# Kernel optimization log

Measured on AMD Instinct MI355X. Metric: run time of the kernel, lower is better.

The kernel has to match this reference:

```python
import jax, jax.numpy as jnp
import numpy as np

N, E, IN, ED, HID, HEADS, OUT, G = 50000, 800000, 128, 16, 32, 4, 64, 64
NEG_SLOPE = 0.2


def gat_conv(x, src, dst, edge_attr, W, att_src, att_dst, We, att_edge, bias,
             heads, out_ch, concat):
    """PyG-style GATConv with edge attributes and mean-filled self loops.
    src/dst already include self loops; edge_attr already includes fill rows."""
    n = x.shape[0]
    h = (x @ W).reshape(n, heads, out_ch)                      # [N,H,C]
    a_src = jnp.einsum('nhc,hc->nh', h, att_src)               # [N,H]
    a_dst = jnp.einsum('nhc,hc->nh', h, att_dst)
    eh = (edge_attr @ We).reshape(-1, heads, out_ch)           # [E',H,C]
    a_edge = jnp.einsum('ehc,hc->eh', eh, att_edge)            # [E',H]
    alpha = jax.nn.leaky_relu(a_src[src] + a_dst[dst] + a_edge, NEG_SLOPE)
    # segment softmax over incoming edges of each target node
    amax = jax.ops.segment_max(alpha, dst, num_segments=n)
    ex = jnp.exp(alpha - amax[dst])
    denom = jax.ops.segment_sum(ex, dst, num_segments=n)
    coef = ex / (denom[dst] + 1e-16)                           # [E',H]
    msg = h[src] * coef[:, :, None]                            # [E',H,C]
    out = jax.ops.segment_sum(msg, dst, num_segments=n)        # [N,H,C]
    out = out.reshape(n, heads * out_ch) if concat else out.mean(axis=1)
    return out + bias


def add_self_loops(edge_index, edge_attr, n):
    loop = jnp.arange(n, dtype=edge_index.dtype)
    src = jnp.concatenate([edge_index[0], loop])
    dst = jnp.concatenate([edge_index[1], loop])
    fill = jnp.broadcast_to(edge_attr.mean(axis=0), (n, edge_attr.shape[1]))
    ea = jnp.concatenate([edge_attr, fill], axis=0)
    return src, dst, ea


def setup_inputs() -> dict:
    key = jax.random.key(0)
    ks = jax.random.split(key, 16)
    s1 = 1.0 / np.sqrt(IN)
    s2 = 1.0 / np.sqrt(HID * HEADS)
    se = 1.0 / np.sqrt(ED)
    return {
        'x': jax.random.normal(ks[0], (N, IN), jnp.float32),
        'edge_index': jax.random.randint(ks[1], (2, E), 0, N, jnp.int64),
        'edge_attr': jax.random.normal(ks[2], (E, ED), jnp.float32),
        'batch': jnp.sort(jax.random.randint(ks[3], (N,), 0, G, jnp.int64)),
        # layer 1 params (heads=4, concat=True)
        'W1': jax.random.normal(ks[4], (IN, HEADS * HID), jnp.float32) * s1,
        'att_src1': jax.random.normal(ks[5], (HEADS, HID), jnp.float32) * s1,
        'att_dst1': jax.random.normal(ks[6], (HEADS, HID), jnp.float32) * s1,
        'We1': jax.random.normal(ks[7], (ED, HEADS * HID), jnp.float32) * se,
        'att_edge1': jax.random.normal(ks[8], (HEADS, HID), jnp.float32) * se,
        'b1': jnp.zeros((HEADS * HID,), jnp.float32),
        # layer 2 params (heads=1, concat=False)
        'W2': jax.random.normal(ks[9], (HEADS * HID, OUT), jnp.float32) * s2,
        'att_src2': jax.random.normal(ks[10], (1, OUT), jnp.float32) * s2,
        'att_dst2': jax.random.normal(ks[11], (1, OUT), jnp.float32) * s2,
        'We2': jax.random.normal(ks[12], (ED, OUT), jnp.float32) * se,
        'att_edge2': jax.random.normal(ks[13], (1, OUT), jnp.float32) * se,
        'b2': jnp.zeros((OUT,), jnp.float32),
    }


def reference(x, edge_index, edge_attr, batch,
              W1, att_src1, att_dst1, We1, att_edge1, b1,
              W2, att_src2, att_dst2, We2, att_edge2, b2):
    src, dst, ea = add_self_loops(edge_index, edge_attr, x.shape[0])
    h = gat_conv(x, src, dst, ea, W1, att_src1, att_dst1, We1, att_edge1, b1,
                 HEADS, HID, concat=True)
    h = jax.nn.elu(h)
    h = gat_conv(h, src, dst, ea, W2, att_src2, att_dst2, We2, att_edge2, b2,
                 1, OUT, concat=False)
    # global mean pool over graphs
    sums = jax.ops.segment_sum(h, batch, num_segments=G)
    cnts = jax.ops.segment_sum(jnp.ones((h.shape[0],), h.dtype), batch, num_segments=G)
    return sums / jnp.maximum(cnts, 1.0)[:, None]
```

## Files before the change

### kernel.cpp

```cpp
#include <hip/hip_runtime.h>
#include <hip/hip_fp16.h>
#include <math.h>

#define NN 50000
#define NE 800000
#define EDF 16
#define C1 128
#define HID 32
#define OUTF 64
#define NG 64
#define SLOPE 0.2f
#define NB 196
#define MAXE 256
#define PB 256
#define PCH 196
#define SEB 512
#define HB 3125
#define G1B 1563
#define G2B 1563

static inline int cdiv(long a, long b){ return (int)((a + b - 1) / b); }

__device__ __forceinline__ float lrelu(float x){ return x >= 0.f ? x : SLOPE * x; }

typedef _Float16 f16x8 __attribute__((ext_vector_type(8)));
typedef float f32x4 __attribute__((ext_vector_type(4)));
#define MFMA16(a, b, c) __builtin_amdgcn_mfma_f32_16x16x32_f16((a), (b), (c), 0, 0, 0)

__global__ __launch_bounds__(256) void k_pre(const float* __restrict__ ea,
                                             float* __restrict__ part,
                                             const int* __restrict__ dst,
                                             int* __restrict__ deg,
                                             int* __restrict__ rank){
  int b = blockIdx.x;
  int t = threadIdx.x;
  if (b < SEB){
    const float4* ea4 = (const float4*)ea;
    const long total = (long)NE * 4;
    const long stride = (long)SEB * 256;
    float4 acc = make_float4(0.f, 0.f, 0.f, 0.f);
    for (long i = (long)b * 256 + t; i < total; i += stride * 4){
      float4 a0 = make_float4(0,0,0,0), a1 = a0, a2 = a0, a3 = a0;
      long i1 = i + stride, i2 = i + 2*stride, i3 = i + 3*stride;
      a0 = ea4[i];
      if (i1 < total) a1 = ea4[i1];
      if (i2 < total) a2 = ea4[i2];
      if (i3 < total) a3 = ea4[i3];
      acc.x += a0.x + a1.x + a2.x + a3.x;
      acc.y += a0.y + a1.y + a2.y + a3.y;
      acc.z += a0.z + a1.z + a2.z + a3.z;
      acc.w += a0.w + a1.w + a2.w + a3.w;
    }
    __shared__ float4 sp[256];
    sp[t] = acc;
    __syncthreads();
    for (int st = 128; st >= 4; st >>= 1){
      if (t < st){
        sp[t].x += sp[t+st].x; sp[t].y += sp[t+st].y;
        sp[t].z += sp[t+st].z; sp[t].w += sp[t+st].w;
      }
      __syncthreads();
    }
    if (t < 4) *(float4*)&part[b * 16 + t * 4] = sp[t];
  } else {
    long e = (long)(b - SEB) * 256 + t;
    if (e < NE) rank[e] = atomicAdd(&deg[dst[e]], 1);
  }
}

__global__ void k_scan1(const int* __restrict__ deg, int* __restrict__ rowStart,
                        int* __restrict__ blockSums,
                        const float* __restrict__ We1, const float* __restrict__ att_e1,
                        const float* __restrict__ We2, const float* __restrict__ att_e2,
                        const float* __restrict__ part,
                        float* __restrict__ M1, float* __restrict__ M2,
                        float* __restrict__ aeSL1, float* __restrict__ aeSL2,
                        const float* __restrict__ W1, const float* __restrict__ W2,
                        __half* __restrict__ W1Th, __half* __restrict__ W1Tl,
                        __half* __restrict__ W2Th, __half* __restrict__ W2Tl){
  int t = threadIdx.x;
  if (blockIdx.x == NB + 1){
    for (int i = t; i < 128 * 128; i += 256){
      int c = i & 127, k = i >> 7;
      float w = W1[i];
      __half h = __float2half_rn(w);
      W1Th[c * 128 + k] = h;
      W1Tl[c * 128 + k] = __float2half_rn((w - __half2float(h)) * 4096.0f);
    }
    return;
  }
  if (blockIdx.x == NB + 2){
    for (int i = t; i < 128 * 64; i += 256){
      int c = i & 63, k = i >> 6;
      float w = W2[i];
      __half h = __float2half_rn(w);
      W2Th[c * 128 + k] = h;
      W2Tl[c * 128 + k] = __float2half_rn((w - __half2float(h)) * 4096.0f);
    }
    return;
  }
  if (blockIdx.x == NB){
    __shared__ float sMean[16];
    __shared__ float sM1p[64];
    if (t < 64){
      int h = t >> 4, d = t & 15;
      float s = 0.f;
      for (int c = 0; c < HID; c++) s += We1[d * C1 + h * HID + c] * att_e1[h * HID + c];
      M1[h * 16 + d] = s; sM1p[t] = s;
    }
    __shared__ float sM2p[16];
    if (t >= 64 && t < 80){
      int d = t - 64;
      float s = 0.f;
      for (int c = 0; c < OUTF; c++) s += We2[d * OUTF + c] * att_e2[c];
      M2[d] = s; sM2p[d] = s;
    }
    if (t >= 80 && t < 96){
      int c = t - 80;
      float s = 0.f;
      for (int b = 0; b < SEB; b++) s += part[b * 16 + c];
      sMean[c] = s * (1.0f / NE);
    }
    __syncthreads();
    if (t < 4){
      float s = 0.f;
      for (int d = 0; d < 16; d++) s += sMean[d] * sM1p[t * 16 + d];
      aeSL1[t] = s;
    }
    if (t == 4){
      float s = 0.f;
      for (int d = 0; d < 16; d++) s += sMean[d] * sM2p[d];
      *aeSL2 = s;
    }
    return;
  }
  __shared__ int sd[256];
  int i = blockIdx.x * 256 + t;
  int v = (i < NN) ? deg[i] : 0;
  sd[t] = v;
  __syncthreads();
  for (int off = 1; off < 256; off <<= 1){
    int add = (t >= off) ? sd[t - off] : 0;
    __syncthreads();
    sd[t] += add;
    __syncthreads();
  }
  int incl = sd[t];
  if (i < NN) rowStart[i] = incl - v;
  if (t == 255) blockSums[blockIdx.x] = incl;
}

__global__ void k_scan3(int* __restrict__ rowStart, const int* __restrict__ blockSums){
  __shared__ int sp[256];
  int t = threadIdx.x;
  int bid = blockIdx.x;
  sp[t] = (t < bid) ? blockSums[t] : 0;
  __syncthreads();
  for (int st = 128; st >= 1; st >>= 1){
    if (t < st) sp[t] += sp[t + st];
    __syncthreads();
  }
  int prefix = sp[0];
  int i = bid * 256 + t;
  if (i < NN) rowStart[i] += prefix;
  if (i == 0) rowStart[NN] = NE;
}

__global__ __launch_bounds__(256) void k_gemm1(
    const float* __restrict__ x,
    const __half* __restrict__ W1Th, const __half* __restrict__ W1Tl,
    __half* __restrict__ Ch,
    const float* __restrict__ attS, const float* __restrict__ attD,
    float* __restrict__ aS, float* __restrict__ aD){
  __shared__ __align__(16) __half Ash[4096];
  __shared__ __align__(16) __half Asl[4096];
  int t = threadIdx.x;
  int row0 = blockIdx.x * 32;
  {
    int srow = t >> 3, sseg = t & 7;
    int gr = row0 + srow;
    float xv[16];
    if (gr < NN){
      const float4* xp = (const float4*)(x + (long)gr * 128 + sseg * 16);
      *(float4*)&xv[0]  = xp[0]; *(float4*)&xv[4]  = xp[1];
      *(float4*)&xv[8]  = xp[2]; *(float4*)&xv[12] = xp[3];
    } else {
#pragma unroll
      for (int i = 0; i < 16; i++) xv[i] = 0.f;
    }
    f16x8 vh[2], vl[2];
#pragma unroll
    for (int q = 0; q < 2; q++)
#pragma unroll
      for (int i = 0; i < 8; i++){
        float f = xv[q * 8 + i];
        _Float16 h = (_Float16)f;
        vh[q][i] = h;
        vl[q][i] = (_Float16)(f - (float)h);
      }
    int sb = srow * 256 + sseg * 32;
    int sw = (srow & 7) << 4;
    *(f16x8*)((char*)Ash + ((sb     ) ^ sw)) = vh[0];
    *(f16x8*)((char*)Ash + ((sb + 16) ^ sw)) = vh[1];
    *(f16x8*)((char*)Asl + ((sb     ) ^ sw)) = vl[0];
    *(f16x8*)((char*)Asl + ((sb + 16) ^ sw)) = vl[1];
  }
  __syncthreads();
  int wave = t >> 6, lane = t & 63, g = lane >> 4, li = lane & 15;
  const f16x8* BhP = (const f16x8*)W1Th;
  const f16x8* BlP = (const f16x8*)W1Tl;
  int c0 = wave * 32 + li;
  int c1 = c0 + 16;
  f32x4 z = {0.f, 0.f, 0.f, 0.f};
  f32x4 aM00 = z, aM01 = z, aM10 = z, aM11 = z;
  f32x4 aL00 = z, aL01 = z, aL10 = z, aL11 = z;
  int ro0 = li * 256, ro1 = (16 + li) * 256;
  int sw0 = (li & 7) << 4;
#pragma unroll
  for (int ks = 0; ks < 4; ks++){
    int ko = ks * 64 + g * 16;
    f16x8 ah0 = *(const f16x8*)((char*)Ash + ((ro0 + ko) ^ sw0));
    f16x8 ah1 = *(const f16x8*)((char*)Ash + ((ro1 + ko) ^ sw0));
    f16x8 al0 = *(const f16x8*)((char*)Asl + ((ro0 + ko) ^ sw0));
    f16x8 al1 = *(const f16x8*)((char*)Asl + ((ro1 + ko) ^ sw0));
    f16x8 bh0 = BhP[c0 * 16 + ks * 4 + g];
    f16x8 bh1 = BhP[c1 * 16 + ks * 4 + g];
    f16x8 bl0 = BlP[c0 * 16 + ks * 4 + g];
    f16x8 bl1 = BlP[c1 * 16 + ks * 4 + g];
    aM00 = MFMA16(ah0, bh0, aM00); aM01 = MFMA16(ah0, bh1, aM01);
    aM10 = MFMA16(ah1, bh0, aM10); aM11 = MFMA16(ah1, bh1, aM11);
    aM00 = MFMA16(al0, bh0, aM00); aM01 = MFMA16(al0, bh1, aM01);
    aM10 = MFMA16(al1, bh0, aM10); aM11 = MFMA16(al1, bh1, aM11);
    aL00 = MFMA16(ah0, bl0, aL00); aL01 = MFMA16(ah0, bl1, aL01);
    aL10 = MFMA16(ah1, bl0, aL10); aL11 = MFMA16(ah1, bl1, aL11);
  }
  const float s = 1.0f / 4096.0f;
  f32x4 D00 = aM00 + aL00 * s, D01 = aM01 + aL01 * s;
  f32x4 D10 = aM10 + aL10 * s, D11 = aM11 + aL11 * s;
  float avS0 = attS[c0], avS1 = attS[c1];
  float avD0 = attD[c0], avD1 = attD[c1];
  float ssv[2][4], sdv[2][4];
#pragma unroll
  for (int r = 0; r < 4; r++){
    ssv[0][r] = D00[r] * avS0 + D01[r] * avS1;
    ssv[1][r] = D10[r] * avS0 + D11[r] * avS1;
    sdv[0][r] = D00[r] * avD0 + D01[r] * avD1;
    sdv[1][r] = D10[r] * avD0 + D11[r] * avD1;
  }
#pragma unroll
  for (int off = 1; off <= 8; off <<= 1)
#pragma unroll
    for (int mt = 0; mt < 2; mt++)
#pragma unroll
      for (int r = 0; r < 4; r++){
        ssv[mt][r] += __shfl_xor(ssv[mt][r], off);
        sdv[mt][r] += __shfl_xor(sdv[mt][r], off);
      }
  __syncthreads();
  __half* sOut = Ash;
#pragma unroll
  for (int mt = 0; mt < 2; mt++)
#pragma unroll
    for (int r = 0; r < 4; r++){
      int rl = mt * 16 + g * 4 + r;
      sOut[rl * 128 + c0] = __float2half_rn(mt ? D10[r] : D00[r]);
      sOut[rl * 128 + c1] = __float2half_rn(mt ? D11[r] : D01[r]);
    }
  if (li == 0){
#pragma unroll
    for (int mt = 0; mt < 2; mt++)
#pragma unroll
      for (int r = 0; r < 4; r++){
        int grow = row0 + mt * 16 + g * 4 + r;
        if (grow < NN){
          aS[(long)grow * 4 + wave] = ssv[mt][r];
          aD[(long)grow * 4 + wave] = sdv[mt][r];
        }
      }
  }
  __syncthreads();
  {
    int row = t >> 3, seg = t & 7;
    int grw = row0 + row;
    if (grw < NN){
      uint4 u0 = *(uint4*)&sOut[row * 128 + seg * 16];
      uint4 u1 = *(uint4*)&sOut[row * 128 + seg * 16 + 8];
      *(uint4*)&Ch[(long)grw * 128 + seg * 16] = u0;
      *(uint4*)&Ch[(long)grw * 128 + seg * 16 + 8] = u1;
    }
  }
}

__global__ __launch_bounds__(256) void k_sc(
    const int* __restrict__ src, const int* __restrict__ dst,
    const float* __restrict__ ea, const int* __restrict__ rowStart,
    const int* __restrict__ rank,
    const float* __restrict__ M1, const float* __restrict__ M2,
    unsigned int* __restrict__ recC){
  __shared__ float sM[80];
  int t = threadIdx.x;
  if (t < 64) sM[t] = M1[t];
  if (t >= 64 && t < 80) sM[t] = M2[t - 64];
  __syncthreads();
  long e = (long)blockIdx.x * 256 + t;
  if (e >= NE) return;
  int d = dst[e];
  int s = src[e];
  int rk = rank[e];
  float eav[16];
  const float4* p = (const float4*)(ea + e * EDF);
  *(float4*)&eav[0]  = p[0]; *(float4*)&eav[4]  = p[1];
  *(float4*)&eav[8]  = p[2]; *(float4*)&eav[12] = p[3];
  int pos = rowStart[d] + rk;
  float ae[4];
#pragma unroll
  for (int h = 0; h < 4; h++){
    float sdot = 0.f;
#pragma unroll
    for (int dd = 0; dd < 16; dd++) sdot += eav[dd] * sM[h * 16 + dd];
    ae[h] = sdot;
  }
  float a2 = 0.f;
#pragma unroll
  for (int dd = 0; dd < 16; dd++) a2 += eav[dd] * sM[64 + dd];
  __half2 ae01 = __floats2half2_rn(ae[0], ae[1]);
  __half2 ae23 = __floats2half2_rn(ae[2], ae[3]);
  __half  a2h  = __float2half_rn(a2);
  uint4 rec;
  rec.x = (unsigned)s | ((unsigned)*(unsigned short*)&a2h << 16);
  rec.y = *(unsigned*)&ae01;
  rec.z = *(unsigned*)&ae23;
  rec.w = 0u;
  *(uint4*)&recC[(long)pos * 4] = rec;
}

__global__ __launch_bounds__(256) void k_gemm2(
    const __half* __restrict__ Ahp,
    const __half* __restrict__ W2Th, const __half* __restrict__ W2Tl,
    __half* __restrict__ Ch,
    const float* __restrict__ attS, const float* __restrict__ attD,
    float* __restrict__ aS, float* __restrict__ aD){
  __shared__ __align__(16) __half As[4096];
  __shared__ float sRS[128], sRD[128];
  int t = threadIdx.x;
  int row0 = blockIdx.x * 32;
  {
    int srow = t >> 3, sseg = t & 7;
    int gr = row0 + srow;
    uint4 u0 = {0,0,0,0}, u1 = {0,0,0,0};
    if (gr < NN){
      const uint4* p = (const uint4*)(Ahp + (long)gr * 128 + sseg * 16);
      u0 = p[0]; u1 = p[1];
    }
    int sb = srow * 256 + sseg * 32;
    int sw = (srow & 7) << 4;
    *(uint4*)((char*)As + ((sb     ) ^ sw)) = u0;
    *(uint4*)((char*)As + ((sb + 16) ^ sw)) = u1;
  }
  __syncthreads();
  int wave = t >> 6, lane = t & 63, g = lane >> 4, li = lane & 15;
  int cw = wave * 16 + li;
  const f16x8* BhP = (const f16x8*)W2Th;
  const f16x8* BlP = (const f16x8*)W2Tl;
  f32x4 z = {0.f, 0.f, 0.f, 0.f};
  f32x4 aM0 = z, aM1 = z, aL0 = z, aL1 = z;
  int ro0 = li * 256, ro1 = (16 + li) * 256, sw0 = (li & 7) << 4;
#pragma unroll
  for (int ks = 0; ks < 4; ks++){
    int ko = ks * 64 + g * 16;
    f16x8 a0 = *(const f16x8*)((char*)As + ((ro0 + ko) ^ sw0));
    f16x8 a1 = *(const f16x8*)((char*)As + ((ro1 + ko) ^ sw0));
    f16x8 bh = BhP[cw * 16 + ks * 4 + g];
    f16x8 bl = BlP[cw * 16 + ks * 4 + g];
    aM0 = MFMA16(a0, bh, aM0); aM1 = MFMA16(a1, bh, aM1);
    aL0 = MFMA16(a0, bl, aL0); aL1 = MFMA16(a1, bl, aL1);
  }
  const float s = 1.0f / 4096.0f;
  f32x4 D0 = aM0 + aL0 * s, D1 = aM1 + aL1 * s;
  float avS = attS[cw], avD = attD[cw];
  float ssv[2][4], sdv[2][4];
#pragma unroll
  for (int r = 0; r < 4; r++){
    ssv[0][r] = D0[r] * avS; ssv[1][r] = D1[r] * avS;
    sdv[0][r] = D0[r] * avD; sdv[1][r] = D1[r] * avD;
  }
#pragma unroll
  for (int off = 1; off <= 8; off <<= 1)
#pragma unroll
    for (int mt = 0; mt < 2; mt++)
#pragma unroll
      for (int r = 0; r < 4; r++){
        ssv[mt][r] += __shfl_xor(ssv[mt][r], off);
        sdv[mt][r] += __shfl_xor(sdv[mt][r], off);
      }
  __syncthreads();
  __half* sOut = As;
#pragma unroll
  for (int mt = 0; mt < 2; mt++)
#pragma unroll
    for (int r = 0; r < 4; r++){
      int rl = mt * 16 + g * 4 + r;
      sOut[rl * 64 + cw] = __float2half_rn(mt ? D1[r] : D0[r]);
      if (li == 0){
        sRS[wave * 32 + rl] = ssv[mt][r];
        sRD[wave * 32 + rl] = sdv[mt][r];
      }
    }
  __syncthreads();
  if (t < 32){
    int grow = row0 + t;
    if (grow < NN){
      aS[grow] = sRS[t] + sRS[32 + t] + sRS[64 + t] + sRS[96 + t];
      aD[grow] = sRD[t] + sRD[32 + t] + sRD[64 + t] + sRD[96 + t];
    }
  }
  {
    int row = t >> 3, seg = t & 7;
    int grw = row0 + row;
    if (grw < NN)
      *(uint4*)&Ch[(long)grw * 64 + seg * 8] = *(uint4*)&sOut[row * 64 + seg * 8];
  }
}

__global__ __launch_bounds__(256) void k_agg1(
    const int* __restrict__ rowStart, const unsigned int* __restrict__ recC,
    const float* __restrict__ a_src, const float* __restrict__ a_dst,
    const float* __restrict__ aeSL1,
    const __half* __restrict__ h1h, const float* __restrict__ b1,
    __half* __restrict__ out1h){
  __shared__ int   sS[4][MAXE];
  __shared__ float sC[4][MAXE * 4];
  int wid = threadIdx.x >> 6;
  int lane = threadIdx.x & 63;
  int n = blockIdx.x * 4 + wid;
  int start = rowStart[n];
  int dg = rowStart[n + 1] - start;
  float4 sl4 = *(const float4*)aeSL1;
  float4 ad4 = *(const float4*)(a_dst + (long)n * 4);
  float4 as4 = *(const float4*)(a_src + (long)n * 4);
  float4 cSelf;
  cSelf.x = __expf(lrelu(as4.x + ad4.x + sl4.x));
  cSelf.y = __expf(lrelu(as4.y + ad4.y + sl4.y));
  cSelf.z = __expf(lrelu(as4.z + ad4.z + sl4.z));
  cSelf.w = __expf(lrelu(as4.w + ad4.w + sl4.w));
  float4 dsum = make_float4(0.f, 0.f, 0.f, 0.f);
  for (int j0 = 0; j0 < dg; j0 += 64){
    int j = j0 + lane;
    if (j < dg){
      uint4 rec = *(const uint4*)&recC[(long)(start + j) * 4];
      int s = rec.x & 0xffff;
      float2 ae01 = __half22float2(*(__half2*)&rec.y);
      float2 ae23 = __half22float2(*(__half2*)&rec.z);
      float4 asv = *(const float4*)(a_src + (long)s * 4);
      float4 c;
      c.x = __expf(lrelu(asv.x + ad4.x + ae01.x));
      c.y = __expf(lrelu(asv.y + ad4.y + ae01.y));
      c.z = __expf(lrelu(asv.z + ad4.z + ae23.x));
      c.w = __expf(lrelu(asv.w + ad4.w + ae23.y));
      dsum.x += c.x; dsum.y += c.y; dsum.z += c.z; dsum.w += c.w;
      if (j < MAXE){
        sS[wid][j] = s << 6;
        *(float4*)&sC[wid][j * 4] = c;
      }
    }
  }
#pragma unroll
  for (int off = 32; off > 0; off >>= 1){
    dsum.x += __shfl_xor(dsum.x, off);
    dsum.y += __shfl_xor(dsum.y, off);
    dsum.z += __shfl_xor(dsum.z, off);
    dsum.w += __shfl_xor(dsum.w, off);
  }
  float adA[4] = {ad4.x, ad4.y, ad4.z, ad4.w};
  float csA[4] = {cSelf.x, cSelf.y, cSelf.z, cSelf.w};
  float invA[4];
  invA[0] = 1.f / (dsum.x + cSelf.x + 1e-16f);
  invA[1] = 1.f / (dsum.y + cSelf.y + 1e-16f);
  invA[2] = 1.f / (dsum.z + cSelf.z + 1e-16f);
  invA[3] = 1.f / (dsum.w + cSelf.w + 1e-16f);
  int ch = lane * 2;
  int h = lane >> 4;
  const unsigned int* hrow = (const unsigned int*)h1h;
  float cs   = csA[h];
  float vinv = invA[h];
  float adh  = adA[h];
  unsigned int hv = hrow[(unsigned)(n * 64 + lane)];
  float2 hf = __half22float2(*(__half2*)&hv);
  float acc0 = hf.x * cs, acc1 = hf.y * cs;
  int jmax = dg < MAXE ? dg : MAXE;
  int j = 0;
  for (; j + 4 <= jmax; j += 4){
    int o0 = sS[wid][j+0], o1 = sS[wid][j+1], o2 = sS[wid][j+2], o3 = sS[wid][j+3];
    float c0 = sC[wid][(j+0)*4+h], c1 = sC[wid][(j+1)*4+h];
    float c2 = sC[wid][(j+2)*4+h], c3 = sC[wid][(j+3)*4+h];
    unsigned int v0 = hrow[(unsigned)(o0 + lane)];
    unsigned int v1 = hrow[(unsigned)(o1 + lane)];
    unsigned int v2 = hrow[(unsigned)(o2 + lane)];
    unsigned int v3 = hrow[(unsigned)(o3 + lane)];
    float2 f0 = __half22float2(*(__half2*)&v0);
    float2 f1 = __half22float2(*(__half2*)&v1);
    float2 f2 = __half22float2(*(__half2*)&v2);
    float2 f3 = __half22float2(*(__half2*)&v3);
    acc0 += c0 * f0.x + c1 * f1.x + c2 * f2.x + c3 * f3.x;
    acc1 += c0 * f0.y + c1 * f1.y + c2 * f2.y + c3 * f3.y;
  }
  for (; j < jmax; j++){
    int o = sS[wid][j];
    float c = sC[wid][j * 4 + h];
    unsigned int v = hrow[(unsigned)(o + lane)];
    float2 f = __half22float2(*(__half2*)&v);
    acc0 += c * f.x; acc1 += c * f.y;
  }
  for (; j < dg; j++){
    uint4 rec = *(const uint4*)&recC[(long)(start + j) * 4];
    int s = rec.x & 0xffff;
    float2 ae01 = __half22float2(*(__half2*)&rec.y);
    float2 ae23 = __half22float2(*(__half2*)&rec.z);
    float aeA[4] = {ae01.x, ae01.y, ae23.x, ae23.y};
    float asv = a_src[(long)s * 4 + h];
    float c = __expf(lrelu(asv + adh + aeA[h]));
    unsigned int v = hrow[(unsigned)((s << 6) + lane)];
    float2 f = __half22float2(*(__half2*)&v);
    acc0 += c * f.x; acc1 += c * f.y;
  }
  float v0 = acc0 * vinv + b1[ch];
  float v1 = acc1 * vinv + b1[ch + 1];
  v0 = v0 > 0.f ? v0 : __expf(v0) - 1.f;
  v1 = v1 > 0.f ? v1 : __expf(v1) - 1.f;
  __half2 pk = __floats2half2_rn(v0, v1);
  ((unsigned int*)out1h)[(unsigned)(n * 64 + lane)] = *(unsigned*)&pk;
}

__global__ __launch_bounds__(256) void k_agg2(
    const int* __restrict__ rowStart, const unsigned int* __restrict__ recC,
    const float* __restrict__ a_src, const float* __restrict__ a_dst,
    const float* __restrict__ aeSL2,
    const __half* __restrict__ h2h, float* __restrict__ out2){
  __shared__ int   sS[4][MAXE];
  __shared__ float sC[4][MAXE];
  int wid = threadIdx.x >> 6;
  int lane = threadIdx.x & 63;
  int n = blockIdx.x * 4 + wid;
  int start = rowStart[n];
  int dg = rowStart[n + 1] - start;
  float adN = a_dst[n];
  float cSelf = __expf(lrelu(a_src[n] + adN + *aeSL2));
  float dsum = 0.f;
  for (int j0 = 0; j0 < dg; j0 += 64){
    int j = j0 + lane;
    if (j < dg){
      unsigned rx = recC[(long)(start + j) * 4];
      int s = rx & 0xffff;
      unsigned short ah = (unsigned short)(rx >> 16);
      float c = __expf(lrelu(a_src[s] + adN + __half2float(*(__half*)&ah)));
      dsum += c;
      if (j < MAXE){ sS[wid][j] = s << 6; sC[wid][j] = c; }
    }
  }
#pragma unroll
  for (int off = 32; off > 0; off >>= 1) dsum += __shfl_xor(dsum, off);
  float inv = 1.f / (dsum + cSelf + 1e-16f);
  float acc = __half2float(h2h[(unsigned)(n * 64 + lane)]) * cSelf;
  int jmax = dg < MAXE ? dg : MAXE;
  int j = 0;
  for (; j + 4 <= jmax; j += 4){
    int o0 = sS[wid][j+0], o1 = sS[wid][j+1], o2 = sS[wid][j+2], o3 = sS[wid][j+3];
    float c0 = sC[wid][j+0], c1 = sC[wid][j+1], c2 = sC[wid][j+2], c3 = sC[wid][j+3];
    float f0 = __half2float(h2h[(unsigned)(o0 + lane)]);
    float f1 = __half2float(h2h[(unsigned)(o1 + lane)]);
    float f2 = __half2float(h2h[(unsigned)(o2 + lane)]);
    float f3 = __half2float(h2h[(unsigned)(o3 + lane)]);
    acc += c0 * f0 + c1 * f1 + c2 * f2 + c3 * f3;
  }
  for (; j < jmax; j++)
    acc += sC[wid][j] * __half2float(h2h[(unsigned)(sS[wid][j] + lane)]);
  for (; j < dg; j++){
    unsigned rx = recC[(long)(start + j) * 4];
    int s = rx & 0xffff;
    unsigned short ah = (unsigned short)(rx >> 16);
    float c = __expf(lrelu(a_src[s] + adN + __half2float(*(__half*)&ah)));
    acc += c * __half2float(h2h[(unsigned)((s << 6) + lane)]);
  }
  out2[(long)n * OUTF + lane] = acc * inv;
}

__global__ __launch_bounds__(256) void k_pool1(const float* __restrict__ out2,
                                               const int* __restrict__ batch,
                                               float* __restrict__ gsum){
  int c = threadIdx.x & 63, r = threadIdx.x >> 6;
  int n0 = blockIdx.x * PCH + r;
  int n1 = blockIdx.x * PCH + PCH; if (n1 > NN) n1 = NN;
  float acc = 0.f; int curG = -1;
  for (int n = n0; n < n1; n += 4){
    int g = batch[n];
    if (g != curG){
      if (curG >= 0) atomicAdd(&gsum[curG * 64 + c], acc);
      curG = g; acc = 0.f;
    }
    acc += out2[(long)n * OUTF + c];
  }
  if (curG >= 0) atomicAdd(&gsum[curG * 64 + c], acc);
}

__global__ void k_pool2(const float* __restrict__ gsum, const int* __restrict__ batch,
                        const float* __restrict__ b2, float* __restrict__ out){
  int g = blockIdx.x;
  int c = threadIdx.x;
  int lo = 0, hi = NN;
  while (lo < hi){ int mid = (lo + hi) >> 1; if (batch[mid] < g) lo = mid + 1; else hi = mid; }
  int a = lo, b = NN;
  while (a < b){ int mid = (a + b) >> 1; if (batch[mid] < g + 1) a = mid + 1; else b = mid; }
  int cnt = a - lo;
  out[g * 64 + c] = (gsum[g * 64 + c] + (float)cnt * b2[c]) / fmaxf((float)cnt, 1.0f);
}

extern "C" void kernel_launch(void* const* d_in, const int* in_sizes, int n_in,
                              void* d_out, int out_size, void* d_ws, size_t ws_size,
                              hipStream_t stream) {
  const float* x         = (const float*)d_in[0];
  const int*   eidx      = (const int*)d_in[1];
  const float* edge_attr = (const float*)d_in[2];
  const int*   batch     = (const int*)d_in[3];
  const float* W1        = (const float*)d_in[4];
  const float* att_src1  = (const float*)d_in[5];
  const float* att_dst1  = (const float*)d_in[6];
  const float* We1       = (const float*)d_in[7];
  const float* att_edge1 = (const float*)d_in[8];
  const float* b1        = (const float*)d_in[9];
  const float* W2        = (const float*)d_in[10];
  const float* att_src2  = (const float*)d_in[11];
  const float* att_dst2  = (const float*)d_in[12];
  const float* We2       = (const float*)d_in[13];
  const float* att_edge2 = (const float*)d_in[14];
  const float* b2        = (const float*)d_in[15];
  const int* srcI = eidx;
  const int* dstI = eidx + NE;

  float* ws = (float*)d_ws;
  __half* h1h   = (__half*)ws;
  __half* out1h = (__half*)(ws + 3200000);
  float* out2   = ws + 6400000;
  float* a_src1 = ws + 9600000;
  float* a_dst1 = a_src1 + (long)NN * 4;
  unsigned int* recC = (unsigned int*)(a_dst1 + (long)NN * 4);
  int*   deg    = (int*)(recC + (long)NE * 4);
  float* gsum   = (float*)(deg + NN);
  int*   rowStart = (int*)(gsum + NG * 64);
  int*   blockSums = rowStart + 50004;
  float* part   = (float*)(blockSums + 260);
  float* M1     = part + SEB * 16;
  float* M2v    = M1 + 64;
  float* aeSL1  = M2v + 16;
  float* aeSL2  = aeSL1 + 4;
  int*   rank   = (int*)(aeSL2 + 4);
  __half* W1Th  = (__half*)(rank + NE);
  __half* W1Tl  = W1Th + 16384;
  __half* W2Th  = W1Tl + 16384;
  __half* W2Tl  = W2Th + 8192;
  __half* h2h = h1h;
  float* a_src2 = a_src1; float* a_dst2 = a_dst1;

  hipMemsetAsync(deg, 0, (NN + NG * 64) * sizeof(int), stream);
  k_pre<<<SEB + HB, 256, 0, stream>>>(edge_attr, part, dstI, deg, rank);
  k_scan1<<<NB + 3, 256, 0, stream>>>(deg, rowStart, blockSums,
                                      We1, att_edge1, We2, att_edge2, part,
                                      M1, M2v, aeSL1, aeSL2,
                                      W1, W2, W1Th, W1Tl, W2Th, W2Tl);
  k_scan3<<<NB, 256, 0, stream>>>(rowStart, blockSums);
  k_gemm1<<<G1B, 256, 0, stream>>>(x, W1Th, W1Tl, h1h, att_src1, att_dst1,
                                   a_src1, a_dst1);
  k_sc<<<HB, 256, 0, stream>>>(srcI, dstI, edge_attr, rowStart, rank,
                               M1, M2v, recC);
  k_agg1<<<NN / 4, 256, 0, stream>>>(rowStart, recC, a_src1, a_dst1, aeSL1,
                                     h1h, b1, out1h);
  k_gemm2<<<G2B, 256, 0, stream>>>(out1h, W2Th, W2Tl, h2h, att_src2, att_dst2,
                                   a_src2, a_dst2);
  k_agg2<<<NN / 4, 256, 0, stream>>>(rowStart, recC, a_src2, a_dst2, aeSL2,
                                     h2h, out2);
  k_pool1<<<PB, 256, 0, stream>>>(out2, batch, gsum);
  k_pool2<<<NG, 64, 0, stream>>>(gsum, batch, b2, (float*)d_out);
}
```

Before: 352.6 us.

## Fuse edge scatter into GEMM1 launch and parallelize weight prep and mean reduction

Merges the edge-record scatter kernel into the first GEMM kernel as extra blocks, so the two independent workloads share one launch and can overlap on the GPU. The weight split/transpose work in the scan kernel is spread over 96 blocks instead of two single-block loops. The edge-attribute mean reduction is parallelized across all 256 threads with a shared-memory reduction. Risks include the larger LDS footprint of the merged kernel for scatter blocks and heavier register pressure that could reduce occupancy.

```diff
diff --git a/kernel.cpp b/kernel.cpp
--- a/kernel.cpp
+++ b/kernel.cpp
@@ -79,18 +79,18 @@
                         __half* __restrict__ W1Th, __half* __restrict__ W1Tl,
                         __half* __restrict__ W2Th, __half* __restrict__ W2Tl){
   int t = threadIdx.x;
-  if (blockIdx.x == NB + 1){
-    for (int i = t; i < 128 * 128; i += 256){
+  int bid = blockIdx.x;
+  if (bid > NB){
+    int wchunk = bid - NB - 1;
+    if (wchunk < 64){
+      int i = wchunk * 256 + t;
       int c = i & 127, k = i >> 7;
       float w = W1[i];
       __half h = __float2half_rn(w);
       W1Th[c * 128 + k] = h;
       W1Tl[c * 128 + k] = __float2half_rn((w - __half2float(h)) * 4096.0f);
-    }
-    return;
-  }
-  if (blockIdx.x == NB + 2){
-    for (int i = t; i < 128 * 64; i += 256){
+    } else {
+      int i = (wchunk - 64) * 256 + t;
       int c = i & 63, k = i >> 6;
       float w = W2[i];
       __half h = __float2half_rn(w);
@@ -99,27 +99,34 @@
     }
     return;
   }
-  if (blockIdx.x == NB){
+  if (bid == NB){
+    __shared__ float red[256];
     __shared__ float sMean[16];
     __shared__ float sM1p[64];
+    __shared__ float sM2p[16];
+    {
+      int c = t & 15, q = t >> 4;
+      float s0 = 0.f;
+      for (int b = q; b < SEB; b += 16) s0 += part[b * 16 + c];
+      red[t] = s0;
+    }
     if (t < 64){
       int h = t >> 4, d = t & 15;
       float s = 0.f;
-      for (int c = 0; c < HID; c++) s += We1[d * C1 + h * HID + c] * att_e1[h * HID + c];
+      for (int cc = 0; cc < HID; cc++) s += We1[d * C1 + h * HID + cc] * att_e1[h * HID + cc];
       M1[h * 16 + d] = s; sM1p[t] = s;
     }
-    __shared__ float sM2p[16];
     if (t >= 64 && t < 80){
       int d = t - 64;
       float s = 0.f;
-      for (int c = 0; c < OUTF; c++) s += We2[d * OUTF + c] * att_e2[c];
+      for (int cc = 0; cc < OUTF; cc++) s += We2[d * OUTF + cc] * att_e2[cc];
       M2[d] = s; sM2p[d] = s;
     }
-    if (t >= 80 && t < 96){
-      int c = t - 80;
-      float s = 0.f;
-      for (int b = 0; b < SEB; b++) s += part[b * 16 + c];
-      sMean[c] = s * (1.0f / NE);
+    __syncthreads();
+    if (t < 16){
+      float m = 0.f;
+      for (int q2 = 0; q2 < 16; q2++) m += red[q2 * 16 + t];
+      sMean[t] = m * (1.0f / NE);
     }
     __syncthreads();
     if (t < 4){
@@ -135,7 +142,7 @@
     return;
   }
   __shared__ int sd[256];
-  int i = blockIdx.x * 256 + t;
+  int i = bid * 256 + t;
   int v = (i < NN) ? deg[i] : 0;
   sd[t] = v;
   __syncthreads();
@@ -147,7 +154,7 @@
   }
   int incl = sd[t];
   if (i < NN) rowStart[i] = incl - v;
-  if (t == 255) blockSums[blockIdx.x] = incl;
+  if (t == 255) blockSums[bid] = incl;
 }
 
 __global__ void k_scan3(int* __restrict__ rowStart, const int* __restrict__ blockSums){
@@ -166,7 +173,12 @@
   if (i == 0) rowStart[NN] = NE;
 }
 
-__global__ __launch_bounds__(256) void k_gemm1(
+__global__ __launch_bounds__(256) void k_sg(
+    const int* __restrict__ src, const int* __restrict__ dst,
+    const float* __restrict__ ea, const int* __restrict__ rowStart,
+    const int* __restrict__ rank,
+    const float* __restrict__ M1, const float* __restrict__ M2,
+    unsigned int* __restrict__ recC,
     const float* __restrict__ x,
     const __half* __restrict__ W1Th, const __half* __restrict__ W1Tl,
     __half* __restrict__ Ch,
@@ -174,7 +186,44 @@
     float* __restrict__ aS, float* __restrict__ aD){
   __shared__ __align__(16) __half Ash[4096];
   __shared__ __align__(16) __half Asl[4096];
+  __shared__ float sM[80];
   int t = threadIdx.x;
+  if ((int)blockIdx.x >= G1B){
+    if (t < 64) sM[t] = M1[t];
+    if (t >= 64 && t < 80) sM[t] = M2[t - 64];
+    __syncthreads();
+    long e = (long)(blockIdx.x - G1B) * 256 + t;
+    if (e >= NE) return;
+    int d = dst[e];
+    int s = src[e];
+    int rk = rank[e];
+    float eav[16];
+    const float4* p = (const float4*)(ea + e * EDF);
+    *(float4*)&eav[0]  = p[0]; *(float4*)&eav[4]  = p[1];
+    *(float4*)&eav[8]  = p[2]; *(float4*)&eav[12] = p[3];
+    int pos = rowStart[d] + rk;
+    float ae[4];
+#pragma unroll
+    for (int h = 0; h < 4; h++){
+      float sdot = 0.f;
+#pragma unroll
+      for (int dd = 0; dd < 16; dd++) sdot += eav[dd] * sM[h * 16 + dd];
+      ae[h] = sdot;
+    }
+    float a2 = 0.f;
+#pragma unroll
+    for (int dd = 0; dd < 16; dd++) a2 += eav[dd] * sM[64 + dd];
+    __half2 ae01 = __floats2half2_rn(ae[0], ae[1]);
+    __half2 ae23 = __floats2half2_rn(ae[2], ae[3]);
+    __half  a2h  = __float2half_rn(a2);
+    uint4 rec;
+    rec.x = (unsigned)s | ((unsigned)*(unsigned short*)&a2h << 16);
+    rec.y = *(unsigned*)&ae01;
+    rec.z = *(unsigned*)&ae23;
+    rec.w = 0u;
+    *(uint4*)&recC[(long)pos * 4] = rec;
+    return;
+  }
   int row0 = blockIdx.x * 32;
   {
     int srow = t >> 3, sseg = t & 7;
@@ -289,49 +338,6 @@
       *(uint4*)&Ch[(long)grw * 128 + seg * 16 + 8] = u1;
     }
   }
-}
-
-__global__ __launch_bounds__(256) void k_sc(
-    const int* __restrict__ src, const int* __restrict__ dst,
-    const float* __restrict__ ea, const int* __restrict__ rowStart,
-    const int* __restrict__ rank,
-    const float* __restrict__ M1, const float* __restrict__ M2,
-    unsigned int* __restrict__ recC){
-  __shared__ float sM[80];
-  int t = threadIdx.x;
-  if (t < 64) sM[t] = M1[t];
-  if (t >= 64 && t < 80) sM[t] = M2[t - 64];
-  __syncthreads();
-  long e = (long)blockIdx.x * 256 + t;
-  if (e >= NE) return;
-  int d = dst[e];
-  int s = src[e];
-  int rk = rank[e];
-  float eav[16];
-  const float4* p = (const float4*)(ea + e * EDF);
-  *(float4*)&eav[0]  = p[0]; *(float4*)&eav[4]  = p[1];
-  *(float4*)&eav[8]  = p[2]; *(float4*)&eav[12] = p[3];
-  int pos = rowStart[d] + rk;
-  float ae[4];
-#pragma unroll
-  for (int h = 0; h < 4; h++){
-    float sdot = 0.f;
-#pragma unroll
-    for (int dd = 0; dd < 16; dd++) sdot += eav[dd] * sM[h * 16 + dd];
-    ae[h] = sdot;
-  }
-  float a2 = 0.f;
-#pragma unroll
-  for (int dd = 0; dd < 16; dd++) a2 += eav[dd] * sM[64 + dd];
-  __half2 ae01 = __floats2half2_rn(ae[0], ae[1]);
-  __half2 ae23 = __floats2half2_rn(ae[2], ae[3]);
-  __half  a2h  = __float2half_rn(a2);
-  uint4 rec;
-  rec.x = (unsigned)s | ((unsigned)*(unsigned short*)&a2h << 16);
-  rec.y = *(unsigned*)&ae01;
-  rec.z = *(unsigned*)&ae23;
-  rec.w = 0u;
-  *(uint4*)&recC[(long)pos * 4] = rec;
 }
 
 __global__ __launch_bounds__(256) void k_gemm2(
@@ -662,15 +668,15 @@
 
   hipMemsetAsync(deg, 0, (NN + NG * 64) * sizeof(int), stream);
   k_pre<<<SEB + HB, 256, 0, stream>>>(edge_attr, part, dstI, deg, rank);
-  k_scan1<<<NB + 3, 256, 0, stream>>>(deg, rowStart, blockSums,
-                                      We1, att_edge1, We2, att_edge2, part,
-                                      M1, M2v, aeSL1, aeSL2,
-                                      W1, W2, W1Th, W1Tl, W2Th, W2Tl);
+  k_scan1<<<NB + 97, 256, 0, stream>>>(deg, rowStart, blockSums,
+                                       We1, att_edge1, We2, att_edge2, part,
+                                       M1, M2v, aeSL1, aeSL2,
+                                       W1, W2, W1Th, W1Tl, W2Th, W2Tl);
   k_scan3<<<NB, 256, 0, stream>>>(rowStart, blockSums);
-  k_gemm1<<<G1B, 256, 0, stream>>>(x, W1Th, W1Tl, h1h, att_src1, att_dst1,
-                                   a_src1, a_dst1);
-  k_sc<<<HB, 256, 0, stream>>>(srcI, dstI, edge_attr, rowStart, rank,
-                               M1, M2v, recC);
+  k_sg<<<G1B + HB, 256, 0, stream>>>(srcI, dstI, edge_attr, rowStart, rank,
+                                     M1, M2v, recC,
+                                     x, W1Th, W1Tl, h1h, att_src1, att_dst1,
+                                     a_src1, a_dst1);
   k_agg1<<<NN / 4, 256, 0, stream>>>(rowStart, recC, a_src1, a_dst1, aeSL1,
                                      h1h, b1, out1h);
   k_gemm2<<<G2B, 256, 0, stream>>>(out1h, W2Th, W2Tl, h2h, att_src2, att_dst2,
```

New measurement: 319.5 us. -9.4%, faster.
